# Kernel optimization log

Measured on AMD Instinct MI355X. Metric: run time of the kernel, lower is better.

## Reference

```python
import jax, jax.numpy as jnp
import numpy as np


def setup_inputs() -> dict:
    key = jax.random.key(0)
    k_f, k_b, k_s, k_c, k_l = jax.random.split(key, 5)
    B, C = 4, 64
    D = H = W = 96
    scale = 4
    Dp = D // scale
    N = 96
    f = jax.random.normal(k_f, (B, C, Dp, Dp, Dp), dtype=jnp.float32)
    inputs = jnp.zeros((B, 1, D, H, W), dtype=jnp.float32)  # only shape is used
    b = jax.random.randint(k_b, (N,), 0, B).astype(jnp.float32)
    score = jax.random.uniform(k_s, (N,), dtype=jnp.float32)
    center = jax.random.uniform(k_c, (N, 3), minval=24.0, maxval=72.0, dtype=jnp.float32)
    side = jax.random.uniform(k_l, (N, 3), minval=16.0, maxval=48.0, dtype=jnp.float32)
    proposals = jnp.concatenate([b[:, None], score[:, None], center, side], axis=1)  # [N, 8]
    return {"f": f, "inputs": inputs, "proposals": proposals,
            "rcnn_crop_size": 7, "scale": scale}


def _pool_axis(x, lo, hi, L, axis, S):
    """Adaptive max-pool one spatial axis of x over per-proposal ranges [lo, hi).

    x: [N, C, ...] with length L at `axis`; lo, hi: [N] int32. Returns x with
    that axis replaced by S adaptive bins (torch adaptive_max_pool semantics:
    bin i covers crop indices [floor(i*Lc/S), ceil((i+1)*Lc/S)) ).
    """
    Lc = hi - lo  # [N] crop length per proposal
    idx = jnp.arange(L, dtype=jnp.int32)  # [L]
    outs = []
    for i in range(S):  # small fixed loop over output bins
        s = lo + (i * Lc) // S
        e = lo + ((i + 1) * Lc + S - 1) // S  # ceil
        mask = (idx[None, :] >= s[:, None]) & (idx[None, :] < e[:, None])  # [N, L]
        shape = [mask.shape[0]] + [1] * (x.ndim - 1)
        shape[axis] = L
        m = mask.reshape(shape)
        outs.append(jnp.max(jnp.where(m, x, -jnp.inf), axis=axis))
    return jnp.stack(outs, axis=axis)


def reference(f, inputs, proposals, rcnn_crop_size, scale):
    S = int(rcnn_crop_size)
    scale = int(scale)
    _, _, Dp, Hp, Wp = f.shape
    # maximum = input spatial dims / scale (feature-space bounds)
    maxdims = jnp.array([d // scale for d in inputs.shape[2:]], dtype=jnp.int32)

    b = proposals[:, 0].astype(jnp.int32)          # [N] batch index
    center = proposals[:, 2:5]                     # [N, 3] (z, y, x)
    side = proposals[:, 5:8]                       # [N, 3]
    c0f = center - side / 2
    c1f = c0f + side
    c0 = jnp.maximum(jnp.floor(c0f / scale).astype(jnp.int32), 0)        # [N, 3]
    c1 = jnp.minimum(jnp.ceil(c1f / scale).astype(jnp.int32), maxdims)   # [N, 3]

    fn = f[b]  # [N, C, Dp, Hp, Wp] per-proposal feature gather
    y = _pool_axis(fn, c0[:, 0], c1[:, 0], Dp, 2, S)  # [N, C, S, Hp, Wp]
    y = _pool_axis(y, c0[:, 1], c1[:, 1], Hp, 3, S)   # [N, C, S, S, Wp]
    y = _pool_axis(y, c0[:, 2], c1[:, 2], Wp, 4, S)   # [N, C, S, S, S]
    return y
```

## Files before the change

kernel.cpp:

```cpp
#include <hip/hip_runtime.h>
#include <hip/hip_fp16.h>


#define SS 7
#define CC 64
#define DP 24
#define DP2 (DP*DP)
#define VOL (DP*DP*DP)
#define INV_SCALE 0.25f
#define NEGINF2 0xFC00FC00u

static __device__ __forceinline__ unsigned pkmax(unsigned a, unsigned b) {
    unsigned r;
    asm("v_pk_max_f16 %0, %1, %2" : "=v"(r) : "v"(a), "v"(b));
    return r;
}
static __device__ __forceinline__ uint4 pkmax4(uint4 a, uint4 b) {
    uint4 r;
    r.x = pkmax(a.x, b.x); r.y = pkmax(a.y, b.y);
    r.z = pkmax(a.z, b.z); r.w = pkmax(a.w, b.w);
    return r;
}

__global__ __launch_bounds__(256) void transpose_cl(
    const float* __restrict__ f,
    uint4* __restrict__ ft4)
{
    __shared__ float tile[64][33];
    const int b  = blockIdx.y;
    const int s0 = blockIdx.x * 32;
    const int t  = threadIdx.x;
    const int x4 = (t & 7) * 4;
    const int rr = t >> 3;
    #pragma unroll
    for (int it = 0; it < 2; ++it) {
        const int r = it * 32 + rr;
        const float4 v = *(const float4*)&f[(size_t)(b * CC + r) * VOL + s0 + x4];
        tile[r][x4 + 0] = v.x; tile[r][x4 + 1] = v.y;
        tile[r][x4 + 2] = v.z; tile[r][x4 + 3] = v.w;
    }
    __syncthreads();
    const int s  = t >> 3;
    const int c8 = (t & 7) * 8;
    __half h[8];
    #pragma unroll
    for (int u = 0; u < 8; ++u)
        h[u] = __float2half(tile[c8 + u][s]);
    ft4[((size_t)b * VOL + s0 + s) * (CC / 8) + (c8 >> 3)] = *(uint4*)h;
}

__global__ __launch_bounds__(256) void croproi_stream(
    const __half* __restrict__ ft,
    const float* __restrict__ props,
    float* __restrict__ out)
{
    __shared__ uint4 P[4 * 104];
    __shared__ float obuf[28 * 68];
    const int n  = blockIdx.x;
    const int i  = blockIdx.y;
    const int zc = blockIdx.z;
    const int t  = threadIdx.x;

    const float* p = props + (size_t)n * 8;
    int b = (int)p[0];
    int lo0, lo1, lo2, L0, L1, L2;
    {
        float c0f = p[2] - 0.5f * p[5];
        float c1f = c0f + p[5];
        int lo = (int)floorf(c0f * INV_SCALE); if (lo < 0) lo = 0;
        int hi = (int)ceilf (c1f * INV_SCALE); if (hi > DP) hi = DP;
        lo0 = lo; L0 = hi - lo;

        c0f = p[3] - 0.5f * p[6];
        c1f = c0f + p[6];
        lo = (int)floorf(c0f * INV_SCALE); if (lo < 0) lo = 0;
        hi = (int)ceilf (c1f * INV_SCALE); if (hi > DP) hi = DP;
        lo1 = lo; L1 = hi - lo;

        c0f = p[4] - 0.5f * p[7];
        c1f = c0f + p[7];
        lo = (int)floorf(c0f * INV_SCALE); if (lo < 0) lo = 0;
        hi = (int)ceilf (c1f * INV_SCALE); if (hi > DP) hi = DP;
        lo2 = lo; L2 = hi - lo;
    }
    b   = __builtin_amdgcn_readfirstlane(b);
    lo0 = __builtin_amdgcn_readfirstlane(lo0);
    lo1 = __builtin_amdgcn_readfirstlane(lo1);
    lo2 = __builtin_amdgcn_readfirstlane(lo2);
    L0  = __builtin_amdgcn_readfirstlane(L0);
    L1  = __builtin_amdgcn_readfirstlane(L1);
    L2  = __builtin_amdgcn_readfirstlane(L2);

    const int zs = (i * L0) / SS;
    const int ez = ((i + 1) * L0 + 6) / SS - zs;
    const int jlo = zc ? 4 : 0;
    const int nj  = zc ? 3 : 4;

    const uint4* base0 = (const uint4*)ft
        + ((size_t)b * VOL + (size_t)(lo0 + zs) * DP2
           + (size_t)lo1 * DP + lo2) * 8;

    const int unitsA = nj * 104;
    for (int u = t; u < unitsA; u += 256) {
        const int jl = u / 104;
        const int r  = u - jl * 104;
        const int x  = r >> 3;
        const int c8 = r & 7;
        const int j  = jlo + jl;
        const int ys = (j * L1) / SS;
        const int ey = ((j + 1) * L1 + 6) / SS - ys;
        const bool act = (x < L2);

        const uint4* bp = base0 + (ys * DP + x) * 8 + c8;
        uint4 m; m.x = m.y = m.z = m.w = NEGINF2;
        #pragma unroll
        for (int zi = 0; zi < 3; ++zi) {
            if (zi < ez) {
                const uint4* bz = bp + zi * (DP2 * 8);
                uint4 v0, v1, v2;
                v0.x = v0.y = v0.z = v0.w = NEGINF2; v1 = v0; v2 = v0;
                if (act)           v0 = bz[0];
                if (act && ey > 1) v1 = bz[DP * 8];
                if (act && ey > 2) v2 = bz[2 * DP * 8];
                m = pkmax4(m, pkmax4(pkmax4(v0, v1), v2));
            }
        }
        if (act) P[jl * 104 + x * 8 + c8] = m;
    }
    __syncthreads();

    const int unitsB = nj * 56;
    if (t < unitsB) {
        const int jkl = t >> 3;
        const int c8  = t & 7;
        const int jl  = jkl / SS;
        const int k   = jkl - jl * SS;
        const int xs  = (k * L2) / SS;
        const int ex  = ((k + 1) * L2 + 6) / SS - xs;
        const uint4* pp = &P[jl * 104 + xs * 8 + c8];
        uint4 m = pp[0];
        if (ex > 1) m = pkmax4(m, pp[8]);
        if (ex > 2) m = pkmax4(m, pp[16]);

        float* o = &obuf[jkl * 68 + c8 * 8];
        __half2 h;
        h = *(const __half2*)&m.x; o[0] = __half2float(h.x); o[1] = __half2float(h.y);
        h = *(const __half2*)&m.y; o[2] = __half2float(h.x); o[3] = __half2float(h.y);
        h = *(const __half2*)&m.z; o[4] = __half2float(h.x); o[5] = __half2float(h.y);
        h = *(const __half2*)&m.w; o[6] = __half2float(h.x); o[7] = __half2float(h.y);
    }
    __syncthreads();

    float* op = out + (size_t)n * CC * (SS * SS * SS) + (size_t)i * 49 + jlo * SS;
    if (zc == 0) {
        for (int idx = t; idx < 28 * CC; idx += 256) {
            const int c = idx / 28;
            const int q = idx - c * 28;
            op[(size_t)c * 343 + q] = obuf[q * 68 + c];
        }
    } else {
        for (int idx = t; idx < 21 * CC; idx += 256) {
            const int c = idx / 21;
            const int q = idx - c * 21;
            op[(size_t)c * 343 + q] = obuf[q * 68 + c];
        }
    }
}

__global__ __launch_bounds__(256) void croproi_fallback(
    const float* __restrict__ f, const float* __restrict__ props,
    float* __restrict__ out, int total)
{
    int tid = blockIdx.x * blockDim.x + threadIdx.x;
    if (tid >= total) return;
    int k = tid % SS;
    int t = tid / SS;
    int j = t % SS; t /= SS;
    int i = t % SS; t /= SS;
    int c = t % CC;
    int n = t / CC;
    const float* p = props + n * 8;
    int b = (int)p[0];
    int lo0, lo1, lo2, L0, L1, L2;
    {
        float c0f = p[2] - 0.5f * p[5]; float c1f = c0f + p[5];
        int lo = (int)floorf(c0f * INV_SCALE); if (lo < 0) lo = 0;
        int hi = (int)ceilf (c1f * INV_SCALE); if (hi > DP) hi = DP;
        lo0 = lo; L0 = hi - lo;
        c0f = p[3] - 0.5f * p[6]; c1f = c0f + p[6];
        lo = (int)floorf(c0f * INV_SCALE); if (lo < 0) lo = 0;
        hi = (int)ceilf (c1f * INV_SCALE); if (hi > DP) hi = DP;
        lo1 = lo; L1 = hi - lo;
        c0f = p[4] - 0.5f * p[7]; c1f = c0f + p[7];
        lo = (int)floorf(c0f * INV_SCALE); if (lo < 0) lo = 0;
        hi = (int)ceilf (c1f * INV_SCALE); if (hi > DP) hi = DP;
        lo2 = lo; L2 = hi - lo;
    }
    int zs = lo0 + (i * L0) / SS, ze = lo0 + ((i + 1) * L0 + SS - 1) / SS;
    int ys = lo1 + (j * L1) / SS, ye = lo1 + ((j + 1) * L1 + SS - 1) / SS;
    int xs = lo2 + (k * L2) / SS, xe = lo2 + ((k + 1) * L2 + SS - 1) / SS;
    const float* fb = f + (size_t)(b * CC + c) * VOL;
    float m = -INFINITY;
    for (int z = zs; z < ze; ++z)
        for (int y = ys; y < ye; ++y) {
            const float* row = fb + (z * DP + y) * DP;
            for (int x = xs; x < xe; ++x) m = fmaxf(m, row[x]);
        }
    out[tid] = m;
}

extern "C" void kernel_launch(void* const* d_in, const int* in_sizes, int n_in,
                              void* d_out, int out_size, void* d_ws, size_t ws_size,
                              hipStream_t stream) {
    const float* f     = (const float*)d_in[0];
    const float* props = (const float*)d_in[2];
    float* out = (float*)d_out;

    const int B = in_sizes[0] / (CC * VOL);
    const int N = in_sizes[2] / 8;

    const size_t ft_bytes = (size_t)B * VOL * CC * sizeof(__half);
    if (ws_size >= ft_bytes) {
        __half* ft = (__half*)d_ws;
        dim3 g1(VOL / 32, B);
        transpose_cl<<<g1, 256, 0, stream>>>(f, (uint4*)ft);
        dim3 g2(N, SS, 2);
        croproi_stream<<<g2, 256, 0, stream>>>(ft, props, out);
    } else {
        int total = N * CC * SS * SS * SS;
        croproi_fallback<<<(total + 255) / 256, 256, 0, stream>>>(f, props, out, total);
    }
}
```

Measured before the change: 17.21 us.

## Split crop blocks by channel halves and pool separably through shared-memory union tile

The second grid dimension now splits channels into two halves instead of splitting output y-bins. Each block first reduces the z-bin over the whole y-x crop region once into a shared tile. It then reduces along y and then along x in shared memory, instead of rereading overlapping y windows from global memory. This removes redundant global loads where adjacent bins overlap. In exchange it adds a third sync stage and more shared memory, and the tile is hard-sized to 13x13, which assumes crop lengths of at most 13.

Result: no change. 17.48 us (+1.6%).

```diff
diff --git a/kernel.cpp b/kernel.cpp
--- a/kernel.cpp
+++ b/kernel.cpp
@@ -49,13 +49,14 @@
     ft4[((size_t)b * VOL + s0 + s) * (CC / 8) + (c8 >> 3)] = *(uint4*)h;
 }
 
-__global__ __launch_bounds__(256) void croproi_stream(
+__global__ __launch_bounds__(256) void croproi_union(
     const __half* __restrict__ ft,
     const float* __restrict__ props,
     float* __restrict__ out)
 {
-    __shared__ uint4 P[4 * 104];
-    __shared__ float obuf[28 * 68];
+    __shared__ uint4 T[13 * 13 * 4];
+    __shared__ uint4 P[7 * 13 * 4];
+    __shared__ float obuf[49 * 33];
     const int n  = blockIdx.x;
     const int i  = blockIdx.y;
     const int zc = blockIdx.z;
@@ -93,56 +94,56 @@
 
     const int zs = (i * L0) / SS;
     const int ez = ((i + 1) * L0 + 6) / SS - zs;
-    const int jlo = zc ? 4 : 0;
-    const int nj  = zc ? 3 : 4;
 
     const uint4* base0 = (const uint4*)ft
         + ((size_t)b * VOL + (size_t)(lo0 + zs) * DP2
-           + (size_t)lo1 * DP + lo2) * 8;
-
-    const int unitsA = nj * 104;
+           + (size_t)lo1 * DP + lo2) * 8 + zc * 4;
+
+    const int unitsA = L1 * L2 * 4;
     for (int u = t; u < unitsA; u += 256) {
-        const int jl = u / 104;
-        const int r  = u - jl * 104;
-        const int x  = r >> 3;
-        const int c8 = r & 7;
-        const int j  = jlo + jl;
-        const int ys = (j * L1) / SS;
-        const int ey = ((j + 1) * L1 + 6) / SS - ys;
-        const bool act = (x < L2);
-
-        const uint4* bp = base0 + (ys * DP + x) * 8 + c8;
-        uint4 m; m.x = m.y = m.z = m.w = NEGINF2;
-        #pragma unroll
-        for (int zi = 0; zi < 3; ++zi) {
-            if (zi < ez) {
-                const uint4* bz = bp + zi * (DP2 * 8);
-                uint4 v0, v1, v2;
-                v0.x = v0.y = v0.z = v0.w = NEGINF2; v1 = v0; v2 = v0;
-                if (act)           v0 = bz[0];
-                if (act && ey > 1) v1 = bz[DP * 8];
-                if (act && ey > 2) v2 = bz[2 * DP * 8];
-                m = pkmax4(m, pkmax4(pkmax4(v0, v1), v2));
-            }
+        const int c8l = u & 3;
+        const int v   = u >> 2;
+        const int y   = v / L2;
+        const int x   = v - y * L2;
+
+        const uint4* bp = base0 + (y * DP + x) * 8 + c8l;
+        uint4 m = bp[0];
+        if (ez > 1) m = pkmax4(m, bp[DP2 * 8]);
+        if (ez > 2) m = pkmax4(m, bp[2 * DP2 * 8]);
+        T[(y * 13 + x) * 4 + c8l] = m;
+    }
+    __syncthreads();
+
+    for (int u = t; u < 7 * 13 * 4; u += 256) {
+        const int c8l = u & 3;
+        const int v   = u >> 2;
+        const int j   = v / 13;
+        const int x   = v - j * 13;
+        if (x < L2) {
+            const int ys = (j * L1) / SS;
+            const int ey = ((j + 1) * L1 + 6) / SS - ys;
+            const uint4* tp = &T[(ys * 13 + x) * 4 + c8l];
+            uint4 m = tp[0];
+            if (ey > 1) m = pkmax4(m, tp[13 * 4]);
+            if (ey > 2) m = pkmax4(m, tp[2 * 13 * 4]);
+            P[(j * 13 + x) * 4 + c8l] = m;
         }
-        if (act) P[jl * 104 + x * 8 + c8] = m;
-    }
-    __syncthreads();
-
-    const int unitsB = nj * 56;
-    if (t < unitsB) {
-        const int jkl = t >> 3;
-        const int c8  = t & 7;
-        const int jl  = jkl / SS;
-        const int k   = jkl - jl * SS;
+    }
+    __syncthreads();
+
+    if (t < 196) {
+        const int jk  = t >> 2;
+        const int c8l = t & 3;
+        const int j   = jk / SS;
+        const int k   = jk - j * SS;
         const int xs  = (k * L2) / SS;
         const int ex  = ((k + 1) * L2 + 6) / SS - xs;
-        const uint4* pp = &P[jl * 104 + xs * 8 + c8];
+        const uint4* pp = &P[(j * 13 + xs) * 4 + c8l];
         uint4 m = pp[0];
-        if (ex > 1) m = pkmax4(m, pp[8]);
-        if (ex > 2) m = pkmax4(m, pp[16]);
-
-        float* o = &obuf[jkl * 68 + c8 * 8];
+        if (ex > 1) m = pkmax4(m, pp[4]);
+        if (ex > 2) m = pkmax4(m, pp[8]);
+
+        float* o = &obuf[jk * 33 + c8l * 8];
         __half2 h;
         h = *(const __half2*)&m.x; o[0] = __half2float(h.x); o[1] = __half2float(h.y);
         h = *(const __half2*)&m.y; o[2] = __half2float(h.x); o[3] = __half2float(h.y);
@@ -151,19 +152,11 @@
     }
     __syncthreads();
 
-    float* op = out + (size_t)n * CC * (SS * SS * SS) + (size_t)i * 49 + jlo * SS;
-    if (zc == 0) {
-        for (int idx = t; idx < 28 * CC; idx += 256) {
-            const int c = idx / 28;
-            const int q = idx - c * 28;
-            op[(size_t)c * 343 + q] = obuf[q * 68 + c];
-        }
-    } else {
-        for (int idx = t; idx < 21 * CC; idx += 256) {
-            const int c = idx / 21;
-            const int q = idx - c * 21;
-            op[(size_t)c * 343 + q] = obuf[q * 68 + c];
-        }
+    float* op = out + ((size_t)n * CC + zc * 32) * (SS * SS * SS) + (size_t)i * 49;
+    for (int idx = t; idx < 32 * 49; idx += 256) {
+        const int c = idx / 49;
+        const int q = idx - c * 49;
+        op[(size_t)c * 343 + q] = obuf[q * 33 + c];
     }
 }
 
@@ -225,7 +218,7 @@
         dim3 g1(VOL / 32, B);
         transpose_cl<<<g1, 256, 0, stream>>>(f, (uint4*)ft);
         dim3 g2(N, SS, 2);
-        croproi_stream<<<g2, 256, 0, stream>>>(ft, props, out);
+        croproi_union<<<g2, 256, 0, stream>>>(ft, props, out);
     } else {
         int total = N * CC * SS * SS * SS;
         croproi_fallback<<<(total + 255) / 256, 256, 0, stream>>>(f, props, out, total);
```
